# Performance work log

Measured on AMD Instinct MI355X. Metric: run time of the kernel, lower is better.

The kernel has to match this reference:

```python
import jax, jax.numpy as jnp
import numpy as np

B = 8            # batch
I_F = 8192       # infeatures
O_F = 8192       # outfeatures
LUT = 8          # 2**3 lookup entries for 3-bit codes
NNZ_PER_ROW = 128
NUMVALS = O_F * NNZ_PER_ROW


def setup_inputs() -> dict:
    key = jax.random.key(0)
    k0, k1, k2, k3, k4 = jax.random.split(key, 5)
    x = jax.random.normal(k0, (B, I_F), dtype=jnp.float32)
    # 3-bit quantized weight codes, one per (in, out) element
    qidx = jax.random.randint(k1, (I_F, O_F), 0, LUT, dtype=jnp.int32)
    # per-output-channel non-uniform quantization lookup table
    lookup_table = jax.random.normal(k2, (O_F, LUT), dtype=jnp.float32)
    # CSR sparse correction: pack2 inserts NNZ_PER_ROW nonzeros per output row
    rows = jnp.arange(O_F + 1, dtype=jnp.int32) * NNZ_PER_ROW
    cols = jax.random.randint(k3, (NUMVALS,), 0, I_F, dtype=jnp.int32)
    vals = jax.random.normal(k4, (NUMVALS,), dtype=jnp.float32)
    return {"x": x, "qidx": qidx, "lookup_table": lookup_table,
            "rows": rows, "cols": cols, "vals": vals}


def reference(x, qidx, lookup_table, rows, cols, vals):
    # Dequantize: W[i, o] = lookup_table[o, qidx[i, o]]   (per-channel NUQ)
    W = lookup_table[jnp.arange(O_F, dtype=jnp.int32)[None, :], qidx]  # (I, O)
    y = x @ W  # (B, O)
    # CSR sparse correction: row id for each nonzero via searchsorted on rows
    seg = jnp.searchsorted(rows[1:], jnp.arange(NUMVALS, dtype=jnp.int32), side="right")
    contrib = vals[None, :] * x[:, cols]                      # (B, numvals)
    y_sp = jax.ops.segment_sum(contrib.T, seg, num_segments=O_F)  # (O, B)
    return y + y_sp.T
```

## Files before the change

kernel.cpp:

```cpp
#include <hip/hip_runtime.h>

#define I_F 8192
#define O_F 8192
#define NSPLIT 64
#define CHUNK (I_F / NSPLIT)

__device__ __forceinline__ float lut_sel(const float4& lo, const float4& hi, int q) {
    const bool b2 = (q & 4) != 0;
    const float s0 = b2 ? hi.x : lo.x;
    const float s1 = b2 ? hi.y : lo.y;
    const float s2 = b2 ? hi.z : lo.z;
    const float s3 = b2 ? hi.w : lo.w;
    const bool b1 = (q & 2) != 0;
    const float t0 = b1 ? s2 : s0;
    const float t1 = b1 ? s3 : s1;
    return (q & 1) ? t1 : t0;
}

__global__ __launch_bounds__(256) void prolog_kernel(const float* __restrict__ x,
                                                     float* __restrict__ xT) {
    const int t = blockIdx.x * 256 + threadIdx.x;
    float4 lo, hi;
    lo.x = x[0 * I_F + t];
    lo.y = x[1 * I_F + t];
    lo.z = x[2 * I_F + t];
    lo.w = x[3 * I_F + t];
    hi.x = x[4 * I_F + t];
    hi.y = x[5 * I_F + t];
    hi.z = x[6 * I_F + t];
    hi.w = x[7 * I_F + t];
    ((float4*)xT)[t * 2]     = lo;
    ((float4*)xT)[t * 2 + 1] = hi;
}

__global__ __launch_bounds__(256) void dense_kernel(const int* __restrict__ qidx,
                                                    const float* __restrict__ lut,
                                                    const float* __restrict__ xT,
                                                    float* __restrict__ P) {
    __shared__ float4 xs[CHUNK][2];

    const int tid = threadIdx.x;
    const int col0 = (blockIdx.x * 256 + tid) * 4;
    const int i0 = blockIdx.y * CHUNK;

    ((float4*)xs)[tid] = ((const float4*)(xT + (size_t)i0 * 8))[tid];

    float4 lA[4], lB[4];
#pragma unroll
    for (int c = 0; c < 4; ++c) {
        const float4* p = (const float4*)(lut + (size_t)(col0 + c) * 8);
        lA[c] = p[0];
        lB[c] = p[1];
    }

    float acc[4][8];
#pragma unroll
    for (int c = 0; c < 4; ++c)
#pragma unroll
        for (int b = 0; b < 8; ++b) acc[c][b] = 0.0f;

    __syncthreads();

    const int4* qp = (const int4*)(qidx + (size_t)i0 * O_F + col0);

#pragma unroll 8
    for (int ii = 0; ii < CHUNK; ++ii) {
        const int4   q   = qp[(size_t)ii * (O_F / 4)];
        const float4 xlo = xs[ii][0];
        const float4 xhi = xs[ii][1];
#pragma unroll
        for (int c = 0; c < 4; ++c) {
            const int qc = (c == 0) ? q.x : (c == 1) ? q.y : (c == 2) ? q.z : q.w;
            const float w = lut_sel(lA[c], lB[c], qc);
            acc[c][0] += xlo.x * w;
            acc[c][1] += xlo.y * w;
            acc[c][2] += xlo.z * w;
            acc[c][3] += xlo.w * w;
            acc[c][4] += xhi.x * w;
            acc[c][5] += xhi.y * w;
            acc[c][6] += xhi.z * w;
            acc[c][7] += xhi.w * w;
        }
    }

    float* Pb = P + ((size_t)blockIdx.y * 8) * O_F + col0;
#pragma unroll
    for (int b = 0; b < 8; ++b) {
        float4 v = make_float4(acc[0][b], acc[1][b], acc[2][b], acc[3][b]);
        *(float4*)(Pb + (size_t)b * O_F) = v;
    }
}

__global__ __launch_bounds__(256) void sparse_kernel(const int* __restrict__ rows,
                                                     const int* __restrict__ cols,
                                                     const float* __restrict__ vals,
                                                     const float* __restrict__ xT,
                                                     float* __restrict__ sp) {
    const int wave = threadIdx.x >> 6;
    const int lane = threadIdx.x & 63;
    const int o = blockIdx.x * 4 + wave;
    const int r0 = rows[o];
    const int r1 = rows[o + 1];

    float acc[8];
#pragma unroll
    for (int b = 0; b < 8; ++b) acc[b] = 0.0f;

    for (int k = r0 + lane; k < r1; k += 64) {
        const int   col = cols[k];
        const float v   = vals[k];
        const float4* xp = (const float4*)(xT + (size_t)col * 8);
        const float4 xlo = xp[0];
        const float4 xhi = xp[1];
        acc[0] += v * xlo.x;
        acc[1] += v * xlo.y;
        acc[2] += v * xlo.z;
        acc[3] += v * xlo.w;
        acc[4] += v * xhi.x;
        acc[5] += v * xhi.y;
        acc[6] += v * xhi.z;
        acc[7] += v * xhi.w;
    }

#pragma unroll
    for (int s = 1; s < 64; s <<= 1)
#pragma unroll
        for (int b = 0; b < 8; ++b) acc[b] += __shfl_xor(acc[b], s, 64);

    if (lane == 0) {
#pragma unroll
        for (int b = 0; b < 8; ++b) sp[(size_t)b * O_F + o] = acc[b];
    }
}

__global__ __launch_bounds__(64) void reduce_kernel(const float* __restrict__ P,
                                                    const float* __restrict__ sp,
                                                    float* __restrict__ out) {
    const int t4 = blockIdx.x * 64 + threadIdx.x;
    float4 s = ((const float4*)sp)[t4];
#pragma unroll 8
    for (int k = 0; k < NSPLIT; ++k) {
        const float4 p = ((const float4*)P)[(size_t)k * (8 * O_F / 4) + t4];
        s.x += p.x; s.y += p.y; s.z += p.z; s.w += p.w;
    }
    ((float4*)out)[t4] = s;
}

extern "C" void kernel_launch(void* const* d_in, const int* in_sizes, int n_in,
                              void* d_out, int out_size, void* d_ws, size_t ws_size,
                              hipStream_t stream) {
    const float* x    = (const float*)d_in[0];
    const int*   qidx = (const int*)d_in[1];
    const float* lut  = (const float*)d_in[2];
    const int*   rows = (const int*)d_in[3];
    const int*   cols = (const int*)d_in[4];
    const float* vals = (const float*)d_in[5];
    float* out = (float*)d_out;

    float* xT = (float*)d_ws;
    float* sp = xT + (size_t)I_F * 8;
    float* P  = sp + (size_t)O_F * 8;

    prolog_kernel<<<I_F / 256, 256, 0, stream>>>(x, xT);
    dense_kernel<<<dim3(O_F / 1024, NSPLIT), 256, 0, stream>>>(qidx, lut, xT, P);
    sparse_kernel<<<O_F / 4, 256, 0, stream>>>(rows, cols, vals, xT, sp);
    reduce_kernel<<<(8 * O_F / 4) / 64, 64, 0, stream>>>(P, sp, out);
}
```

Before: 400.7 us.

## Pack LUT to fp16 in prolog and retile dense kernel to 8 columns per thread

The prolog now converts the per-channel lookup table to packed fp16 (four uint32 per output column), cutting LUT register footprint so each thread can handle 8 output columns. The dense kernel is retiled to 1024-thread blocks covering all 8192 columns, with 256 input splits of 32 rows each, reading two int4 qidx vectors per row. The reduce kernel must now sum 256 partials instead of 64, quadrupling partial-buffer traffic. fp16 LUT values add rounding error.

```diff
diff --git a/kernel.cpp b/kernel.cpp
--- a/kernel.cpp
+++ b/kernel.cpp
@@ -1,24 +1,15 @@
 #include <hip/hip_runtime.h>
+#include <hip/hip_fp16.h>
 
 #define I_F 8192
 #define O_F 8192
-#define NSPLIT 64
-#define CHUNK (I_F / NSPLIT)
-
-__device__ __forceinline__ float lut_sel(const float4& lo, const float4& hi, int q) {
-    const bool b2 = (q & 4) != 0;
-    const float s0 = b2 ? hi.x : lo.x;
-    const float s1 = b2 ? hi.y : lo.y;
-    const float s2 = b2 ? hi.z : lo.z;
-    const float s3 = b2 ? hi.w : lo.w;
-    const bool b1 = (q & 2) != 0;
-    const float t0 = b1 ? s2 : s0;
-    const float t1 = b1 ? s3 : s1;
-    return (q & 1) ? t1 : t0;
-}
+#define NSPLIT 256
+#define RPB 32
 
 __global__ __launch_bounds__(256) void prolog_kernel(const float* __restrict__ x,
-                                                     float* __restrict__ xT) {
+                                                     const float* __restrict__ lut,
+                                                     float* __restrict__ xT,
+                                                     uint4* __restrict__ lutH) {
     const int t = blockIdx.x * 256 + threadIdx.x;
     float4 lo, hi;
     lo.x = x[0 * I_F + t];
@@ -31,47 +22,63 @@
     hi.w = x[7 * I_F + t];
     ((float4*)xT)[t * 2]     = lo;
     ((float4*)xT)[t * 2 + 1] = hi;
+
+    const float4* lp = (const float4*)(lut + (size_t)t * 8);
+    const float4 l0 = lp[0];
+    const float4 l1 = lp[1];
+    uint4 h;
+    h.x = (unsigned)__half_as_ushort(__float2half_rn(l0.x)) |
+          ((unsigned)__half_as_ushort(__float2half_rn(l0.y)) << 16);
+    h.y = (unsigned)__half_as_ushort(__float2half_rn(l0.z)) |
+          ((unsigned)__half_as_ushort(__float2half_rn(l0.w)) << 16);
+    h.z = (unsigned)__half_as_ushort(__float2half_rn(l1.x)) |
+          ((unsigned)__half_as_ushort(__float2half_rn(l1.y)) << 16);
+    h.w = (unsigned)__half_as_ushort(__float2half_rn(l1.z)) |
+          ((unsigned)__half_as_ushort(__float2half_rn(l1.w)) << 16);
+    lutH[t] = h;
 }
 
-__global__ __launch_bounds__(256) void dense_kernel(const int* __restrict__ qidx,
-                                                    const float* __restrict__ lut,
-                                                    const float* __restrict__ xT,
-                                                    float* __restrict__ P) {
-    __shared__ float4 xs[CHUNK][2];
+__global__ __launch_bounds__(1024, 4) void dense_kernel(const int* __restrict__ qidx,
+                                                        const uint4* __restrict__ lutH,
+                                                        const float* __restrict__ xT,
+                                                        float* __restrict__ P) {
+    __shared__ float4 xs[RPB][2];
 
     const int tid = threadIdx.x;
-    const int col0 = (blockIdx.x * 256 + tid) * 4;
-    const int i0 = blockIdx.y * CHUNK;
+    const int split = blockIdx.x;
+    const int i0 = split * RPB;
+    const int col0 = tid * 8;
 
-    ((float4*)xs)[tid] = ((const float4*)(xT + (size_t)i0 * 8))[tid];
+    if (tid < RPB * 2)
+        ((float4*)xs)[tid] = ((const float4*)(xT + (size_t)i0 * 8))[tid];
 
-    float4 lA[4], lB[4];
+    uint4 lh[8];
 #pragma unroll
-    for (int c = 0; c < 4; ++c) {
-        const float4* p = (const float4*)(lut + (size_t)(col0 + c) * 8);
-        lA[c] = p[0];
-        lB[c] = p[1];
-    }
+    for (int c = 0; c < 8; ++c) lh[c] = lutH[col0 + c];
 
-    float acc[4][8];
+    float acc[8][8];
 #pragma unroll
-    for (int c = 0; c < 4; ++c)
+    for (int c = 0; c < 8; ++c)
 #pragma unroll
         for (int b = 0; b < 8; ++b) acc[c][b] = 0.0f;
 
     __syncthreads();
 
-    const int4* qp = (const int4*)(qidx + (size_t)i0 * O_F + col0);
+    const int4* qp = (const int4*)(qidx + (size_t)i0 * O_F) + tid * 2;
 
-#pragma unroll 8
-    for (int ii = 0; ii < CHUNK; ++ii) {
-        const int4   q   = qp[(size_t)ii * (O_F / 4)];
-        const float4 xlo = xs[ii][0];
-        const float4 xhi = xs[ii][1];
+    for (int r = 0; r < RPB; ++r) {
+        const int4 qa = qp[(size_t)r * (O_F / 4)];
+        const int4 qb = qp[(size_t)r * (O_F / 4) + 1];
+        const float4 xlo = xs[r][0];
+        const float4 xhi = xs[r][1];
 #pragma unroll
-        for (int c = 0; c < 4; ++c) {
-            const int qc = (c == 0) ? q.x : (c == 1) ? q.y : (c == 2) ? q.z : q.w;
-            const float w = lut_sel(lA[c], lB[c], qc);
+        for (int c = 0; c < 8; ++c) {
+            const int q = (c < 4) ? ((c == 0) ? qa.x : (c == 1) ? qa.y : (c == 2) ? qa.z : qa.w)
+                                  : ((c == 4) ? qb.x : (c == 5) ? qb.y : (c == 6) ? qb.z : qb.w);
+            const unsigned a = (q & 4) ? ((q & 2) ? lh[c].w : lh[c].z)
+                                       : ((q & 2) ? lh[c].y : lh[c].x);
+            const unsigned sel = (q & 1) ? (a >> 16) : (a & 0xffffu);
+            const float w = __half2float(__ushort_as_half((unsigned short)sel));
             acc[c][0] += xlo.x * w;
             acc[c][1] += xlo.y * w;
             acc[c][2] += xlo.z * w;
@@ -83,11 +90,11 @@
         }
     }
 
-    float* Pb = P + ((size_t)blockIdx.y * 8) * O_F + col0;
+    float* Pb = P + ((size_t)split * 8) * O_F + col0;
 #pragma unroll
     for (int b = 0; b < 8; ++b) {
-        float4 v = make_float4(acc[0][b], acc[1][b], acc[2][b], acc[3][b]);
-        *(float4*)(Pb + (size_t)b * O_F) = v;
+        *(float4*)(Pb + (size_t)b * O_F)     = make_float4(acc[0][b], acc[1][b], acc[2][b], acc[3][b]);
+        *(float4*)(Pb + (size_t)b * O_F + 4) = make_float4(acc[4][b], acc[5][b], acc[6][b], acc[7][b]);
     }
 }
 
@@ -133,10 +140,10 @@
     }
 }
 
-__global__ __launch_bounds__(64) void reduce_kernel(const float* __restrict__ P,
-                                                    const float* __restrict__ sp,
-                                                    float* __restrict__ out) {
-    const int t4 = blockIdx.x * 64 + threadIdx.x;
+__global__ __launch_bounds__(128) void reduce_kernel(const float* __restrict__ P,
+                                                     const float* __restrict__ sp,
+                                                     float* __restrict__ out) {
+    const int t4 = blockIdx.x * 128 + threadIdx.x;
     float4 s = ((const float4*)sp)[t4];
 #pragma unroll 8
     for (int k = 0; k < NSPLIT; ++k) {
@@ -157,12 +164,13 @@
     const float* vals = (const float*)d_in[5];
     float* out = (float*)d_out;
 
-    float* xT = (float*)d_ws;
-    float* sp = xT + (size_t)I_F * 8;
-    float* P  = sp + (size_t)O_F * 8;
+    float* xT   = (float*)d_ws;
+    float* sp   = xT + (size_t)I_F * 8;
+    uint4* lutH = (uint4*)(sp + (size_t)O_F * 8);
+    float* P    = (float*)(lutH + O_F);
 
-    prolog_kernel<<<I_F / 256, 256, 0, stream>>>(x, xT);
-    dense_kernel<<<dim3(O_F / 1024, NSPLIT), 256, 0, stream>>>(qidx, lut, xT, P);
+    prolog_kernel<<<I_F / 256, 256, 0, stream>>>(x, lut, xT, lutH);
+    dense_kernel<<<NSPLIT, 1024, 0, stream>>>(qidx, lutH, xT, P);
     sparse_kernel<<<O_F / 4, 256, 0, stream>>>(rows, cols, vals, xT, sp);
-    reduce_kernel<<<(8 * O_F / 4) / 64, 64, 0, stream>>>(P, sp, out);
+    reduce_kernel<<<(8 * O_F / 4) / 128, 128, 0, stream>>>(P, sp, out);
 }
```

New measurement: 417.0 us. 4.1% more time.
